# Kernel tuning notes

Hardware: AMD Instinct MI355X
Metric: run time of the kernel (lower is better)

Reference implementation:

```python
import jax, jax.numpy as jnp
import numpy as np

N = 100000      # nodes (words + docs)
E = 1600000     # edges
D_IN = 256      # input feature dim
H = 64          # hidden dim
C = 20          # num classes
NDOC = 10000    # doc nodes


def setup_inputs() -> dict:
    key = jax.random.key(0)
    ks = jax.random.split(key, 16)
    inp = {
        "x": jax.random.normal(ks[0], (N, D_IN), dtype=jnp.float32),
        "edge_weight": jax.random.uniform(ks[1], (E,), dtype=jnp.float32),
        "W1": jax.random.normal(ks[2], (D_IN, H), dtype=jnp.float32) * (1.0 / np.sqrt(D_IN)),
        "b1": jnp.zeros((H,), jnp.float32),
        "W2": jax.random.normal(ks[3], (H, H), dtype=jnp.float32) * (1.0 / np.sqrt(H)),
        "b2": jnp.zeros((H,), jnp.float32),
        "W3": jax.random.normal(ks[4], (H, H), dtype=jnp.float32) * (1.0 / np.sqrt(H)),
        "b3": jnp.zeros((H,), jnp.float32),
        "Wp": jax.random.normal(ks[5], (H, H), dtype=jnp.float32) * (1.0 / np.sqrt(H)),
        "bp": jnp.zeros((H,), jnp.float32),
        "Wc": jax.random.normal(ks[6], (H, C), dtype=jnp.float32) * (1.0 / np.sqrt(H)),
        "bc": jnp.zeros((C,), jnp.float32),
        "edge_index": jax.random.randint(ks[7], (2, E), 0, N, dtype=jnp.int32),
        "doc_idx": jnp.sort(jax.random.randint(ks[8], (NDOC,), 0, N, dtype=jnp.int32)),
    }
    return inp


def reference(x, edge_weight, W1, b1, W2, b2, W3, b3, Wp, bp, Wc, bc, edge_index, doc_idx):
    n = x.shape[0]
    src, dst = edge_index[0], edge_index[1]
    loop = jnp.arange(n, dtype=src.dtype)
    rows = jnp.concatenate([src, loop])          # sources (incl. self-loops)
    cols = jnp.concatenate([dst, loop])          # targets
    w = jnp.concatenate([edge_weight, jnp.ones((n,), x.dtype)])
    # symmetric GCN normalization: D^-1/2 (A + I) D^-1/2
    deg = jax.ops.segment_sum(w, cols, num_segments=n)
    deg_safe = jnp.where(deg > 0, deg, 1.0)
    dinv = jnp.where(deg > 0, jax.lax.rsqrt(deg_safe), 0.0)
    norm = dinv[rows] * w * dinv[cols]           # [E+N]

    def conv(h, W, b):
        h = h @ W                                # transform first (PyG GCNConv)
        msg = h[rows] * norm[:, None]            # gather + weight  [E+N, H]
        return jax.ops.segment_sum(msg, cols, num_segments=n) + b

    h = jax.nn.relu(conv(x, W1, b1))             # dropout = identity (eval mode)
    h = jax.nn.relu(conv(h, W2, b2))
    h = jax.nn.relu(conv(h, W3, b3))
    d = h[doc_idx]                               # [NDOC, H]
    d = jax.nn.relu(d @ Wp + bp)
    return d @ Wc + bc                           # [NDOC, C]
```

## Files before the change

### kernel.cpp

```cpp
#include <hip/hip_runtime.h>

#define H 64
#define PAD 48
#define WFIX 262144.0f
#define WFIX_INV (1.0f / 262144.0f)


__global__ __launch_bounds__(256) void k_init(unsigned int* packed, int n) {
    int i = blockIdx.x * 256 + threadIdx.x;
    if (i < n) packed[i] = 0u;
}


__global__ __launch_bounds__(256) void k_fused(const int* __restrict__ src,
                                               const int* __restrict__ dst,
                                               const float* __restrict__ ew,
                                               unsigned int* packed,
                                               int2* __restrict__ csr,
                                               int e_total,
                                               const float* __restrict__ A,
                                               const float* __restrict__ B,
                                               float* __restrict__ out, int M) {
    __shared__ float As[64][68];
    __shared__ float Bs[64][64];
    int tid = threadIdx.x;

    const int K = 256;
    int brow = blockIdx.x * 64;
    int ct = tid & 15, rt = tid >> 4;
    int c4 = ct * 4, r4 = rt * 4;
    int lrow = tid >> 4;
    int lk4 = (tid & 15) * 4;
    float acc[4][4] = {{0.f}};

    int ebase = blockIdx.x * 1024 + tid;

    for (int t4 = 0; t4 < 4; ++t4) {
        int k0 = t4 * 64;
        int e = ebase + t4 * 256;
        bool ok = e < e_total;
        int ed = 0, es = 0; float w = 0.f;
        if (ok) { ed = dst[e]; es = src[e]; w = ew[e]; }

#pragma unroll
        for (int rr = 0; rr < 64; rr += 16) {
            int row = brow + rr + lrow;
            float4 va = make_float4(0.f, 0.f, 0.f, 0.f);
            if (row < M) va = *(const float4*)&A[(size_t)row * K + k0 + lk4];
            *(float4*)&As[rr + lrow][lk4] = va;
            float4 vb = *(const float4*)&B[(size_t)(k0 + rr + lrow) * 64 + lk4];
            *(float4*)&Bs[rr + lrow][lk4] = vb;
        }
        __syncthreads();

        unsigned int old = 0;
        if (ok) {
            unsigned int enc = (1u << 24) | (unsigned int)(w * WFIX + 0.5f);
            old = atomicAdd(&packed[ed], enc);
        }

#pragma unroll 16
        for (int kk = 0; kk < 64; ++kk) {
            float4 bv = *(const float4*)&Bs[kk][c4];
#pragma unroll
            for (int i = 0; i < 4; ++i) {
                float av = As[r4 + i][kk];
                acc[i][0] = fmaf(av, bv.x, acc[i][0]);
                acc[i][1] = fmaf(av, bv.y, acc[i][1]);
                acc[i][2] = fmaf(av, bv.z, acc[i][2]);
                acc[i][3] = fmaf(av, bv.w, acc[i][3]);
            }
        }

        if (ok) {
            unsigned int r = old >> 24;
            if (r < PAD) csr[(size_t)ed * PAD + r] = make_int2(es, __float_as_int(w));
        }
        __syncthreads();
    }

#pragma unroll
    for (int i = 0; i < 4; ++i) {
        int row = brow + r4 + i;
        if (row < M)
            *(float4*)&out[(size_t)row * H + c4] =
                make_float4(acc[i][0], acc[i][1], acc[i][2], acc[i][3]);
    }
}


__global__ __launch_bounds__(256) void k_dinv(const unsigned int* __restrict__ packed,
                                              float* __restrict__ dinv, int n) {
    int i = blockIdx.x * 256 + threadIdx.x;
    if (i < n) {
        unsigned int pv = packed[i];
        dinv[i] = rsqrtf(1.0f + (float)(pv & 0xFFFFFFu) * WFIX_INV);
    }
}


#define XRED4(a)  { a.x += __shfl_xor(a.x, 16, 64); a.y += __shfl_xor(a.y, 16, 64); \
                    a.z += __shfl_xor(a.z, 16, 64); a.w += __shfl_xor(a.w, 16, 64); \
                    a.x += __shfl_xor(a.x, 32, 64); a.y += __shfl_xor(a.y, 32, 64); \
                    a.z += __shfl_xor(a.z, 32, 64); a.w += __shfl_xor(a.w, 32, 64); }

__global__ __launch_bounds__(256) void k_agg(const float* __restrict__ t,
                                             float* __restrict__ h,
                                             const int2* __restrict__ csr,
                                             const unsigned int* __restrict__ packed,
                                             const float* __restrict__ dinv,
                                             const float* __restrict__ bias, int n) {
    int wid = (int)((blockIdx.x * 256u + threadIdx.x) >> 6);
    int lane = threadIdx.x & 63;
    if (wid >= n) return;
    int g = lane >> 4;
    int s = lane & 15;
    float di = dinv[wid];
    int cnt = (int)(packed[wid] >> 24);
    if (cnt > PAD) cnt = PAD;
    const int2* row = &csr[(size_t)wid * PAD];
    float4 acc = make_float4(0.f, 0.f, 0.f, 0.f);
    int j = 0;
    for (; j + 4 <= cnt; j += 4) {
        int2 en = row[j + g];
        float m = __int_as_float(en.y) * dinv[en.x];
        float4 v = *(const float4*)&t[(size_t)en.x * H + s * 4];
        acc.x = fmaf(v.x, m, acc.x);
        acc.y = fmaf(v.y, m, acc.y);
        acc.z = fmaf(v.z, m, acc.z);
        acc.w = fmaf(v.w, m, acc.w);
    }
    if (j + g < cnt) {
        int2 en = row[j + g];
        float m = __int_as_float(en.y) * dinv[en.x];
        float4 v = *(const float4*)&t[(size_t)en.x * H + s * 4];
        acc.x = fmaf(v.x, m, acc.x);
        acc.y = fmaf(v.y, m, acc.y);
        acc.z = fmaf(v.z, m, acc.z);
        acc.w = fmaf(v.w, m, acc.w);
    }
    XRED4(acc);
    if (g == 0) {
        float4 self4 = *(const float4*)&t[(size_t)wid * H + s * 4];
        float4 b4 = *(const float4*)&bias[s * 4];
        float dd = di * di;
        float4 o;
        o.x = fmaxf(fmaf(di, acc.x, fmaf(dd, self4.x, b4.x)), 0.f);
        o.y = fmaxf(fmaf(di, acc.y, fmaf(dd, self4.y, b4.y)), 0.f);
        o.z = fmaxf(fmaf(di, acc.z, fmaf(dd, self4.z, b4.z)), 0.f);
        o.w = fmaxf(fmaf(di, acc.w, fmaf(dd, self4.w, b4.w)), 0.f);
        *(float4*)&h[(size_t)wid * H + s * 4] = o;
    }
}


__global__ __launch_bounds__(256) void k_aggdoc(const float* __restrict__ t,
                                                float* __restrict__ dbuf,
                                                const int2* __restrict__ csr,
                                                const unsigned int* __restrict__ packed,
                                                const float* __restrict__ dinv,
                                                const float* __restrict__ bias,
                                                const int* __restrict__ doc, int ndoc) {
    int wid = (int)((blockIdx.x * 256u + threadIdx.x) >> 6);
    int lane = threadIdx.x & 63;
    if (wid >= ndoc) return;
    int g = lane >> 4;
    int s = lane & 15;
    int d = doc[wid];
    float di = dinv[d];
    int cnt = (int)(packed[d] >> 24);
    if (cnt > PAD) cnt = PAD;
    const int2* row = &csr[(size_t)d * PAD];
    float4 acc = make_float4(0.f, 0.f, 0.f, 0.f);
    int j = 0;
    for (; j + 4 <= cnt; j += 4) {
        int2 en = row[j + g];
        float m = __int_as_float(en.y) * dinv[en.x];
        float4 v = *(const float4*)&t[(size_t)en.x * H + s * 4];
        acc.x = fmaf(v.x, m, acc.x);
        acc.y = fmaf(v.y, m, acc.y);
        acc.z = fmaf(v.z, m, acc.z);
        acc.w = fmaf(v.w, m, acc.w);
    }
    if (j + g < cnt) {
        int2 en = row[j + g];
        float m = __int_as_float(en.y) * dinv[en.x];
        float4 v = *(const float4*)&t[(size_t)en.x * H + s * 4];
        acc.x = fmaf(v.x, m, acc.x);
        acc.y = fmaf(v.y, m, acc.y);
        acc.z = fmaf(v.z, m, acc.z);
        acc.w = fmaf(v.w, m, acc.w);
    }
    XRED4(acc);
    if (g == 0) {
        float4 self4 = *(const float4*)&t[(size_t)d * H + s * 4];
        float4 b4 = *(const float4*)&bias[s * 4];
        float dd = di * di;
        float4 o;
        o.x = fmaxf(fmaf(di, acc.x, fmaf(dd, self4.x, b4.x)), 0.f);
        o.y = fmaxf(fmaf(di, acc.y, fmaf(dd, self4.y, b4.y)), 0.f);
        o.z = fmaxf(fmaf(di, acc.z, fmaf(dd, self4.z, b4.z)), 0.f);
        o.w = fmaxf(fmaf(di, acc.w, fmaf(dd, self4.w, b4.w)), 0.f);
        *(float4*)&dbuf[(size_t)wid * H + s * 4] = o;
    }
}


__global__ __launch_bounds__(256) void k_gemm64(const float* __restrict__ A,
                                                const float* __restrict__ B,
                                                float* __restrict__ out, int M) {
    __shared__ float As[64][68];
    __shared__ float Bs[64][64];
    int tid = threadIdx.x;
    int brow = blockIdx.x * 64;
    int ct = tid & 15, rt = tid >> 4;
    int c4 = ct * 4, r4 = rt * 4;
    int lrow = tid >> 4;
    int lk4 = (tid & 15) * 4;
    float acc[4][4] = {{0.f}};

#pragma unroll
    for (int rr = 0; rr < 64; rr += 16) {
        int row = brow + rr + lrow;
        float4 va = make_float4(0.f, 0.f, 0.f, 0.f);
        if (row < M) va = *(const float4*)&A[(size_t)row * H + lk4];
        *(float4*)&As[rr + lrow][lk4] = va;
        float4 vb = *(const float4*)&B[(size_t)(rr + lrow) * 64 + lk4];
        *(float4*)&Bs[rr + lrow][lk4] = vb;
    }
    __syncthreads();
#pragma unroll 16
    for (int kk = 0; kk < 64; ++kk) {
        float4 bv = *(const float4*)&Bs[kk][c4];
#pragma unroll
        for (int i = 0; i < 4; ++i) {
            float av = As[r4 + i][kk];
            acc[i][0] = fmaf(av, bv.x, acc[i][0]);
            acc[i][1] = fmaf(av, bv.y, acc[i][1]);
            acc[i][2] = fmaf(av, bv.z, acc[i][2]);
            acc[i][3] = fmaf(av, bv.w, acc[i][3]);
        }
    }
#pragma unroll
    for (int i = 0; i < 4; ++i) {
        int row = brow + r4 + i;
        if (row < M)
            *(float4*)&out[(size_t)row * H + c4] =
                make_float4(acc[i][0], acc[i][1], acc[i][2], acc[i][3]);
    }
}


__global__ __launch_bounds__(256) void k_docgemm(const float* __restrict__ dbuf,
                                                 const float* __restrict__ Wp,
                                                 const float* __restrict__ bp,
                                                 const float* __restrict__ Wc,
                                                 const float* __restrict__ bc,
                                                 float* __restrict__ out,
                                                 int m, int ncls) {
    __shared__ float As[64][68];
    __shared__ float Bs[64][64];
    int tid = threadIdx.x;
    int brow = blockIdx.x * 64;
    int ct = tid & 15, rt = tid >> 4;
    int c4 = ct * 4, r4 = rt * 4;
    int lrow = tid >> 4;
    int lk4 = (tid & 15) * 4;
    float acc[4][4] = {{0.f}};

#pragma unroll
    for (int rr = 0; rr < 64; rr += 16) {
        int row = brow + rr + lrow;
        float4 va = make_float4(0.f, 0.f, 0.f, 0.f);
        if (row < m) va = *(const float4*)&dbuf[(size_t)row * H + lk4];
        *(float4*)&As[rr + lrow][lk4] = va;
        float4 vb = *(const float4*)&Wp[(size_t)(rr + lrow) * 64 + lk4];
        *(float4*)&Bs[rr + lrow][lk4] = vb;
    }
    __syncthreads();
#pragma unroll 16
    for (int kk = 0; kk < 64; ++kk) {
        float4 bv = *(const float4*)&Bs[kk][c4];
#pragma unroll
        for (int i = 0; i < 4; ++i) {
            float av = As[r4 + i][kk];
            acc[i][0] = fmaf(av, bv.x, acc[i][0]);
            acc[i][1] = fmaf(av, bv.y, acc[i][1]);
            acc[i][2] = fmaf(av, bv.z, acc[i][2]);
            acc[i][3] = fmaf(av, bv.w, acc[i][3]);
        }
    }
    __syncthreads();

#pragma unroll
    for (int i = 0; i < 4; ++i) {
        float4 v = make_float4(acc[i][0] + bp[c4],     acc[i][1] + bp[c4 + 1],
                               acc[i][2] + bp[c4 + 2], acc[i][3] + bp[c4 + 3]);
        v.x = fmaxf(v.x, 0.f); v.y = fmaxf(v.y, 0.f);
        v.z = fmaxf(v.z, 0.f); v.w = fmaxf(v.w, 0.f);
        *(float4*)&Bs[r4 + i][c4] = v;
    }
    float* wcs = &As[0][0];
    float* bcs = &As[32][0];
    for (int i = tid; i < H * ncls; i += 256) wcs[i] = Wc[i];
    if (tid < ncls) bcs[tid] = bc[tid];
    __syncthreads();

    for (int o = tid; o < 64 * ncls; o += 256) {
        int r = o / ncls, c = o % ncls;
        int grow = brow + r;
        if (grow >= m) continue;
        float a = bcs[c];
#pragma unroll
        for (int k = 0; k < H; ++k) a = fmaf(Bs[r][k], wcs[k * ncls + c], a);
        out[(size_t)grow * ncls + c] = a;
    }
}


extern "C" void kernel_launch(void* const* d_in, const int* in_sizes, int n_in,
                              void* d_out, int out_size, void* d_ws, size_t ws_size,
                              hipStream_t stream) {
    const float* x  = (const float*)d_in[0];
    const float* ew = (const float*)d_in[1];
    const float* W1 = (const float*)d_in[2];
    const float* b1 = (const float*)d_in[3];
    const float* W2 = (const float*)d_in[4];
    const float* b2 = (const float*)d_in[5];
    const float* W3 = (const float*)d_in[6];
    const float* b3 = (const float*)d_in[7];
    const float* Wp = (const float*)d_in[8];
    const float* bp = (const float*)d_in[9];
    const float* Wc = (const float*)d_in[10];
    const float* bc = (const float*)d_in[11];
    const int*   ei = (const int*)d_in[12];
    const int*  doc = (const int*)d_in[13];
    float* out = (float*)d_out;

    const int DIN  = 256;
    const int n    = in_sizes[0] / DIN;
    const int e    = in_sizes[1];
    const int ndoc = in_sizes[13];
    const int ncls = 20;

    const int* src = ei;
    const int* dst = ei + e;

    char* p = (char*)d_ws;
    auto alloc = [&](size_t bytes) { char* r = p; p += (bytes + 255) & ~(size_t)255; return r; };
    unsigned int* packed = (unsigned int*)alloc((size_t)n * 4);
    float*        dinv   = (float*)alloc((size_t)n * 4);
    int2*         csr    = (int2*)alloc((size_t)n * PAD * 8);
    float*        tbuf   = (float*)alloc((size_t)n * H * 4);
    float*        hbuf   = (float*)alloc((size_t)n * H * 4);
    float*        dbuf   = (float*)alloc((size_t)ndoc * H * 4);

    int nb_n = (n + 255) / 256;
    int nb_g = (n + 63) / 64;
    int nb_a = (n + 3) / 4;
    int nb_ad = (ndoc + 3) / 4;
    int nb_d  = (ndoc + 63) / 64;

    k_init<<<nb_n, 256, 0, stream>>>(packed, n);
    k_fused<<<nb_g, 256, 0, stream>>>(src, dst, ew, packed, csr, e, x, W1, tbuf, n);
    k_dinv<<<nb_n, 256, 0, stream>>>(packed, dinv, n);
    k_agg<<<nb_a, 256, 0, stream>>>(tbuf, hbuf, csr, packed, dinv, b1, n);
    k_gemm64<<<nb_g, 256, 0, stream>>>(hbuf, W2, tbuf, n);
    k_agg<<<nb_a, 256, 0, stream>>>(tbuf, hbuf, csr, packed, dinv, b2, n);
    k_gemm64<<<nb_g, 256, 0, stream>>>(hbuf, W3, tbuf, n);
    k_aggdoc<<<nb_ad, 256, 0, stream>>>(tbuf, dbuf, csr, packed, dinv, b3, doc, ndoc);
    k_docgemm<<<nb_d, 256, 0, stream>>>(dbuf, Wp, bp, Wc, bc, out, ndoc, ncls);
}
```

Measured before the change: 477.6 us.

## Fuse neighbor aggregation with following dense GEMM and unroll gather loop

Merges each aggregation kernel with the next layer's 64x64 weight GEMM: each block aggregates 64 nodes into shared memory (16 nodes per wave, processed serially), then multiplies them by the weight tile. The document path likewise fuses its aggregation with the classifier GEMMs. This removes the intermediate h buffer write and read plus several launches. The gather loop is also unrolled by two edges per lane group so more loads are in flight. The trade-off is fewer waves per node: 100k nodes now map to about 1.5k blocks instead of 25k, with each wave walking 16 nodes in sequence, which can cut the latency hiding the gather depends on.

```diff
diff --git a/kernel.cpp b/kernel.cpp
--- a/kernel.cpp
+++ b/kernel.cpp
@@ -98,137 +98,100 @@
     }
 }
 
-
 #define XRED4(a)  { a.x += __shfl_xor(a.x, 16, 64); a.y += __shfl_xor(a.y, 16, 64); \
                     a.z += __shfl_xor(a.z, 16, 64); a.w += __shfl_xor(a.w, 16, 64); \
                     a.x += __shfl_xor(a.x, 32, 64); a.y += __shfl_xor(a.y, 32, 64); \
                     a.z += __shfl_xor(a.z, 32, 64); a.w += __shfl_xor(a.w, 32, 64); }
 
-__global__ __launch_bounds__(256) void k_agg(const float* __restrict__ t,
-                                             float* __restrict__ h,
-                                             const int2* __restrict__ csr,
-                                             const unsigned int* __restrict__ packed,
-                                             const float* __restrict__ dinv,
-                                             const float* __restrict__ bias, int n) {
-    int wid = (int)((blockIdx.x * 256u + threadIdx.x) >> 6);
-    int lane = threadIdx.x & 63;
-    if (wid >= n) return;
-    int g = lane >> 4;
-    int s = lane & 15;
-    float di = dinv[wid];
-    int cnt = (int)(packed[wid] >> 24);
+__device__ __forceinline__ float4 agg_node(int node,
+                                           const float* __restrict__ t,
+                                           const int2* __restrict__ csr,
+                                           const unsigned int* __restrict__ packed,
+                                           const float* __restrict__ dinv,
+                                           const float* __restrict__ bias,
+                                           int g, int s) {
+    float di = dinv[node];
+    int cnt = (int)(packed[node] >> 24);
     if (cnt > PAD) cnt = PAD;
-    const int2* row = &csr[(size_t)wid * PAD];
+    const int2* row = &csr[(size_t)node * PAD];
     float4 acc = make_float4(0.f, 0.f, 0.f, 0.f);
     int j = 0;
-    for (; j + 4 <= cnt; j += 4) {
+    for (; j + 8 <= cnt; j += 8) {
+        int2 ea = row[j + g];
+        int2 eb = row[j + 4 + g];
+        float4 va = *(const float4*)&t[(size_t)ea.x * H + s * 4];
+        float4 vb = *(const float4*)&t[(size_t)eb.x * H + s * 4];
+        float ma = __int_as_float(ea.y) * dinv[ea.x];
+        float mb = __int_as_float(eb.y) * dinv[eb.x];
+        acc.x = fmaf(va.x, ma, acc.x); acc.y = fmaf(va.y, ma, acc.y);
+        acc.z = fmaf(va.z, ma, acc.z); acc.w = fmaf(va.w, ma, acc.w);
+        acc.x = fmaf(vb.x, mb, acc.x); acc.y = fmaf(vb.y, mb, acc.y);
+        acc.z = fmaf(vb.z, mb, acc.z); acc.w = fmaf(vb.w, mb, acc.w);
+    }
+    if (j + 4 <= cnt) {
         int2 en = row[j + g];
         float m = __int_as_float(en.y) * dinv[en.x];
         float4 v = *(const float4*)&t[(size_t)en.x * H + s * 4];
-        acc.x = fmaf(v.x, m, acc.x);
-        acc.y = fmaf(v.y, m, acc.y);
-        acc.z = fmaf(v.z, m, acc.z);
-        acc.w = fmaf(v.w, m, acc.w);
+        acc.x = fmaf(v.x, m, acc.x); acc.y = fmaf(v.y, m, acc.y);
+        acc.z = fmaf(v.z, m, acc.z); acc.w = fmaf(v.w, m, acc.w);
+        j += 4;
     }
     if (j + g < cnt) {
         int2 en = row[j + g];
         float m = __int_as_float(en.y) * dinv[en.x];
         float4 v = *(const float4*)&t[(size_t)en.x * H + s * 4];
-        acc.x = fmaf(v.x, m, acc.x);
-        acc.y = fmaf(v.y, m, acc.y);
-        acc.z = fmaf(v.z, m, acc.z);
-        acc.w = fmaf(v.w, m, acc.w);
+        acc.x = fmaf(v.x, m, acc.x); acc.y = fmaf(v.y, m, acc.y);
+        acc.z = fmaf(v.z, m, acc.z); acc.w = fmaf(v.w, m, acc.w);
     }
     XRED4(acc);
+    float4 o = make_float4(0.f, 0.f, 0.f, 0.f);
     if (g == 0) {
-        float4 self4 = *(const float4*)&t[(size_t)wid * H + s * 4];
+        float4 self4 = *(const float4*)&t[(size_t)node * H + s * 4];
         float4 b4 = *(const float4*)&bias[s * 4];
         float dd = di * di;
-        float4 o;
         o.x = fmaxf(fmaf(di, acc.x, fmaf(dd, self4.x, b4.x)), 0.f);
         o.y = fmaxf(fmaf(di, acc.y, fmaf(dd, self4.y, b4.y)), 0.f);
         o.z = fmaxf(fmaf(di, acc.z, fmaf(dd, self4.z, b4.z)), 0.f);
         o.w = fmaxf(fmaf(di, acc.w, fmaf(dd, self4.w, b4.w)), 0.f);
-        *(float4*)&h[(size_t)wid * H + s * 4] = o;
-    }
-}
-
-
-__global__ __launch_bounds__(256) void k_aggdoc(const float* __restrict__ t,
-                                                float* __restrict__ dbuf,
-                                                const int2* __restrict__ csr,
-                                                const unsigned int* __restrict__ packed,
-                                                const float* __restrict__ dinv,
-                                                const float* __restrict__ bias,
-                                                const int* __restrict__ doc, int ndoc) {
-    int wid = (int)((blockIdx.x * 256u + threadIdx.x) >> 6);
-    int lane = threadIdx.x & 63;
-    if (wid >= ndoc) return;
-    int g = lane >> 4;
-    int s = lane & 15;
-    int d = doc[wid];
-    float di = dinv[d];
-    int cnt = (int)(packed[d] >> 24);
-    if (cnt > PAD) cnt = PAD;
-    const int2* row = &csr[(size_t)d * PAD];
-    float4 acc = make_float4(0.f, 0.f, 0.f, 0.f);
-    int j = 0;
-    for (; j + 4 <= cnt; j += 4) {
-        int2 en = row[j + g];
-        float m = __int_as_float(en.y) * dinv[en.x];
-        float4 v = *(const float4*)&t[(size_t)en.x * H + s * 4];
-        acc.x = fmaf(v.x, m, acc.x);
-        acc.y = fmaf(v.y, m, acc.y);
-        acc.z = fmaf(v.z, m, acc.z);
-        acc.w = fmaf(v.w, m, acc.w);
-    }
-    if (j + g < cnt) {
-        int2 en = row[j + g];
-        float m = __int_as_float(en.y) * dinv[en.x];
-        float4 v = *(const float4*)&t[(size_t)en.x * H + s * 4];
-        acc.x = fmaf(v.x, m, acc.x);
-        acc.y = fmaf(v.y, m, acc.y);
-        acc.z = fmaf(v.z, m, acc.z);
-        acc.w = fmaf(v.w, m, acc.w);
-    }
-    XRED4(acc);
-    if (g == 0) {
-        float4 self4 = *(const float4*)&t[(size_t)d * H + s * 4];
-        float4 b4 = *(const float4*)&bias[s * 4];
-        float dd = di * di;
-        float4 o;
-        o.x = fmaxf(fmaf(di, acc.x, fmaf(dd, self4.x, b4.x)), 0.f);
-        o.y = fmaxf(fmaf(di, acc.y, fmaf(dd, self4.y, b4.y)), 0.f);
-        o.z = fmaxf(fmaf(di, acc.z, fmaf(dd, self4.z, b4.z)), 0.f);
-        o.w = fmaxf(fmaf(di, acc.w, fmaf(dd, self4.w, b4.w)), 0.f);
-        *(float4*)&dbuf[(size_t)wid * H + s * 4] = o;
-    }
-}
-
-
-__global__ __launch_bounds__(256) void k_gemm64(const float* __restrict__ A,
-                                                const float* __restrict__ B,
-                                                float* __restrict__ out, int M) {
+    }
+    return o;
+}
+
+
+__global__ __launch_bounds__(256) void k_fuseagg(const float* __restrict__ t,
+                                                 float* __restrict__ tn,
+                                                 const int2* __restrict__ csr,
+                                                 const unsigned int* __restrict__ packed,
+                                                 const float* __restrict__ dinv,
+                                                 const float* __restrict__ bias,
+                                                 const float* __restrict__ W, int n) {
     __shared__ float As[64][68];
     __shared__ float Bs[64][64];
     int tid = threadIdx.x;
     int brow = blockIdx.x * 64;
+    int lrow = tid >> 4;
+    int lk4 = (tid & 15) * 4;
+
+#pragma unroll
+    for (int rr = 0; rr < 64; rr += 16) {
+        float4 vb = *(const float4*)&W[(size_t)(rr + lrow) * 64 + lk4];
+        *(float4*)&Bs[rr + lrow][lk4] = vb;
+    }
+
+    int wv = tid >> 6;
+    int lane = tid & 63;
+    int g = lane >> 4, s = lane & 15;
+    for (int i = 0; i < 16; ++i) {
+        int node = brow + wv * 16 + i;
+        float4 o = make_float4(0.f, 0.f, 0.f, 0.f);
+        if (node < n) o = agg_node(node, t, csr, packed, dinv, bias, g, s);
+        if (g == 0) *(float4*)&As[wv * 16 + i][s * 4] = o;
+    }
+    __syncthreads();
+
     int ct = tid & 15, rt = tid >> 4;
     int c4 = ct * 4, r4 = rt * 4;
-    int lrow = tid >> 4;
-    int lk4 = (tid & 15) * 4;
     float acc[4][4] = {{0.f}};
-
-#pragma unroll
-    for (int rr = 0; rr < 64; rr += 16) {
-        int row = brow + rr + lrow;
-        float4 va = make_float4(0.f, 0.f, 0.f, 0.f);
-        if (row < M) va = *(const float4*)&A[(size_t)row * H + lk4];
-        *(float4*)&As[rr + lrow][lk4] = va;
-        float4 vb = *(const float4*)&B[(size_t)(rr + lrow) * 64 + lk4];
-        *(float4*)&Bs[rr + lrow][lk4] = vb;
-    }
-    __syncthreads();
 #pragma unroll 16
     for (int kk = 0; kk < 64; ++kk) {
         float4 bv = *(const float4*)&Bs[kk][c4];
@@ -244,40 +207,52 @@
 #pragma unroll
     for (int i = 0; i < 4; ++i) {
         int row = brow + r4 + i;
-        if (row < M)
-            *(float4*)&out[(size_t)row * H + c4] =
+        if (row < n)
+            *(float4*)&tn[(size_t)row * H + c4] =
                 make_float4(acc[i][0], acc[i][1], acc[i][2], acc[i][3]);
     }
 }
 
 
-__global__ __launch_bounds__(256) void k_docgemm(const float* __restrict__ dbuf,
-                                                 const float* __restrict__ Wp,
-                                                 const float* __restrict__ bp,
-                                                 const float* __restrict__ Wc,
-                                                 const float* __restrict__ bc,
-                                                 float* __restrict__ out,
-                                                 int m, int ncls) {
+__global__ __launch_bounds__(256) void k_docall(const float* __restrict__ t,
+                                                const int2* __restrict__ csr,
+                                                const unsigned int* __restrict__ packed,
+                                                const float* __restrict__ dinv,
+                                                const float* __restrict__ b3,
+                                                const float* __restrict__ Wp,
+                                                const float* __restrict__ bp,
+                                                const float* __restrict__ Wc,
+                                                const float* __restrict__ bc,
+                                                const int* __restrict__ doc,
+                                                float* __restrict__ out,
+                                                int m, int ncls) {
     __shared__ float As[64][68];
     __shared__ float Bs[64][64];
     int tid = threadIdx.x;
     int brow = blockIdx.x * 64;
+    int lrow = tid >> 4;
+    int lk4 = (tid & 15) * 4;
+
+#pragma unroll
+    for (int rr = 0; rr < 64; rr += 16) {
+        float4 vb = *(const float4*)&Wp[(size_t)(rr + lrow) * 64 + lk4];
+        *(float4*)&Bs[rr + lrow][lk4] = vb;
+    }
+
+    int wv = tid >> 6;
+    int lane = tid & 63;
+    int g = lane >> 4, s = lane & 15;
+    for (int i = 0; i < 16; ++i) {
+        int r = brow + wv * 16 + i;
+        float4 o = make_float4(0.f, 0.f, 0.f, 0.f);
+        if (r < m) o = agg_node(doc[r], t, csr, packed, dinv, b3, g, s);
+        if (g == 0) *(float4*)&As[wv * 16 + i][s * 4] = o;
+    }
+    __syncthreads();
+
     int ct = tid & 15, rt = tid >> 4;
     int c4 = ct * 4, r4 = rt * 4;
-    int lrow = tid >> 4;
-    int lk4 = (tid & 15) * 4;
     float acc[4][4] = {{0.f}};
-
-#pragma unroll
-    for (int rr = 0; rr < 64; rr += 16) {
-        int row = brow + rr + lrow;
-        float4 va = make_float4(0.f, 0.f, 0.f, 0.f);
-        if (row < m) va = *(const float4*)&dbuf[(size_t)row * H + lk4];
-        *(float4*)&As[rr + lrow][lk4] = va;
-        float4 vb = *(const float4*)&Wp[(size_t)(rr + lrow) * 64 + lk4];
-        *(float4*)&Bs[rr + lrow][lk4] = vb;
-    }
-    __syncthreads();
 #pragma unroll 16
     for (int kk = 0; kk < 64; ++kk) {
         float4 bv = *(const float4*)&Bs[kk][c4];
@@ -352,22 +327,17 @@
     float*        dinv   = (float*)alloc((size_t)n * 4);
     int2*         csr    = (int2*)alloc((size_t)n * PAD * 8);
     float*        tbuf   = (float*)alloc((size_t)n * H * 4);
-    float*        hbuf   = (float*)alloc((size_t)n * H * 4);
-    float*        dbuf   = (float*)alloc((size_t)ndoc * H * 4);
+    float*        ubuf   = (float*)alloc((size_t)n * H * 4);
 
     int nb_n = (n + 255) / 256;
     int nb_g = (n + 63) / 64;
-    int nb_a = (n + 3) / 4;
-    int nb_ad = (ndoc + 3) / 4;
-    int nb_d  = (ndoc + 63) / 64;
+    int nb_d = (ndoc + 63) / 64;
 
     k_init<<<nb_n, 256, 0, stream>>>(packed, n);
     k_fused<<<nb_g, 256, 0, stream>>>(src, dst, ew, packed, csr, e, x, W1, tbuf, n);
     k_dinv<<<nb_n, 256, 0, stream>>>(packed, dinv, n);
-    k_agg<<<nb_a, 256, 0, stream>>>(tbuf, hbuf, csr, packed, dinv, b1, n);
-    k_gemm64<<<nb_g, 256, 0, stream>>>(hbuf, W2, tbuf, n);
-    k_agg<<<nb_a, 256, 0, stream>>>(tbuf, hbuf, csr, packed, dinv, b2, n);
-    k_gemm64<<<nb_g, 256, 0, stream>>>(hbuf, W3, tbuf, n);
-    k_aggdoc<<<nb_ad, 256, 0, stream>>>(tbuf, dbuf, csr, packed, dinv, b3, doc, ndoc);
-    k_docgemm<<<nb_d, 256, 0, stream>>>(dbuf, Wp, bp, Wc, bc, out, ndoc, ncls);
-}
+    k_fuseagg<<<nb_g, 256, 0, stream>>>(tbuf, ubuf, csr, packed, dinv, b1, W2, n);
+    k_fuseagg<<<nb_g, 256, 0, stream>>>(ubuf, tbuf, csr, packed, dinv, b2, W3, n);
+    k_docall<<<nb_d, 256, 0, stream>>>(tbuf, csr, packed, dinv, b3, Wp, bp, Wc, bc,
+                                       doc, out, ndoc, ncls);
+}
```

Measured after the change: 601.8 us. 26.0% more time.
